# Optimization experiments

Hardware: AMD Instinct MI355X
Metric: run time of the kernel (lower is better)

Reference implementation:

```python
import jax, jax.numpy as jnp
import numpy as np

T_START = 0.0
T_END = 1.0
STEPS = 10
HID = 1024
BATCH = 8192


def setup_inputs() -> dict:
    key = jax.random.key(0)
    ks = jax.random.split(key, 7)
    s1 = 1.0 / np.sqrt(HID + 1)
    s2 = 1.0 / np.sqrt(HID)
    return {
        "h": jax.random.normal(ks[0], (BATCH, HID), dtype=jnp.float32),
        "W1": jax.random.uniform(ks[1], (HID + 1, HID), jnp.float32, -s1, s1),
        "b1": jax.random.uniform(ks[2], (HID,), jnp.float32, -s1, s1),
        "W2": jax.random.uniform(ks[3], (HID, HID), jnp.float32, -s2, s2),
        "b2": jax.random.uniform(ks[4], (HID,), jnp.float32, -s2, s2),
        "W3": jax.random.uniform(ks[5], (HID, HID), jnp.float32, -s2, s2),
        "b3": jax.random.uniform(ks[6], (HID,), jnp.float32, -s2, s2),
    }


def reference(h, W1, b1, W2, b2, W3, b3):
    dt = (T_END - T_START) / STEPS

    def dynamics(t, h):
        # concat(h, t*ones) @ W1 == h @ W1[:-1] + t * W1[-1]; keep explicit concat for clarity
        t_vec = jnp.full((h.shape[0], 1), t, dtype=h.dtype)
        x = jnp.concatenate([h, t_vec], axis=1)
        x = jnp.tanh(x @ W1 + b1)
        x = jnp.tanh(x @ W2 + b2)
        return x @ W3 + b3

    def rk4_step(h, t):
        k1 = dynamics(t, h)
        k2 = dynamics(t + dt / 2, h + dt / 2 * k1)
        k3 = dynamics(t + dt / 2, h + dt / 2 * k2)
        k4 = dynamics(t + dt, h + dt * k3)
        return h + dt / 6 * (k1 + 2 * k2 + 2 * k3 + k4), None

    ts = T_START + dt * jnp.arange(STEPS, dtype=h.dtype)
    h_final, _ = jax.lax.scan(rk4_step, h, ts)
    return h_final
```

## Files before the change

kernel.cpp:

```cpp
#include <hip/hip_runtime.h>


typedef __attribute__((ext_vector_type(8))) __bf16 bf16x8;
typedef __attribute__((ext_vector_type(4))) float f32x4;
typedef __attribute__((ext_vector_type(8))) float f32x8;
typedef __attribute__((ext_vector_type(16))) float f32x16;
typedef __attribute__((ext_vector_type(8))) unsigned short us8;
typedef __attribute__((ext_vector_type(4))) int i32x4;
typedef __attribute__((ext_vector_type(8))) int i32x8;
typedef unsigned short ushort_t;
typedef unsigned char u8;

#define SCALE_ONE  0x7F7F7F7Fu
#define SCALE_INV32 0x7A7A7A7Au

#define GLOAD16(gp, lp) \
  __builtin_amdgcn_global_load_lds((const __attribute__((address_space(1))) unsigned int*)(gp), \
                                   (__attribute__((address_space(3))) unsigned int*)(lp), 16, 0, 0)

__device__ __forceinline__ ushort_t f2bf(float f) {
  union { float f; unsigned u; } v; v.f = f;
  unsigned r = v.u + 0x7fffu + ((v.u >> 16) & 1u);
  return (ushort_t)(r >> 16);
}
__device__ __forceinline__ float b2f(ushort_t u) {
  union { unsigned u; float f; } v; v.u = ((unsigned)u) << 16; return v.f;
}
__device__ __forceinline__ float fast_tanh(float x) {
  float e = __expf(2.0f * x);
  return 1.0f - 2.0f * __builtin_amdgcn_rcpf(e + 1.0f);
}
__device__ __forceinline__ uint2 pack_fp8x8(const float* v) {
  int a = __builtin_amdgcn_cvt_pk_fp8_f32(v[0], v[1], 0, false);
  a = __builtin_amdgcn_cvt_pk_fp8_f32(v[2], v[3], a, true);
  int b = __builtin_amdgcn_cvt_pk_fp8_f32(v[4], v[5], 0, false);
  b = __builtin_amdgcn_cvt_pk_fp8_f32(v[6], v[7], b, true);
  return make_uint2((unsigned)a, (unsigned)b);
}

__global__ void transpose_bf16(const float* __restrict__ in, ushort_t* __restrict__ out) {
  __shared__ float tile[32][33];
  const int bx = blockIdx.x * 32, by = blockIdx.y * 32;
  const int tx = threadIdx.x, ty = threadIdx.y;
#pragma unroll
  for (int i = 0; i < 32; i += 8)
    tile[ty + i][tx] = in[(size_t)(by + ty + i) * 1024 + bx + tx];
  __syncthreads();
#pragma unroll
  for (int i = 0; i < 32; i += 8)
    out[(size_t)(bx + ty + i) * 1024 + by + tx] = f2bf(tile[tx][ty + i]);
}

__global__ void transpose_fp8(const float* __restrict__ in, u8* __restrict__ out) {
  __shared__ float tile[32][33];
  const int bx = blockIdx.x * 32, by = blockIdx.y * 32;
  const int tx = threadIdx.x, ty = threadIdx.y;
#pragma unroll
  for (int i = 0; i < 32; i += 8)
    tile[ty + i][tx] = in[(size_t)(by + ty + i) * 1024 + bx + tx];
  __syncthreads();
#pragma unroll
  for (int i = 0; i < 32; i += 8) {
    const float v = 32.f * tile[tx][ty + i];
    int r = __builtin_amdgcn_cvt_pk_fp8_f32(v, v, 0, false);
    out[(size_t)(bx + ty + i) * 1024 + by + tx] = (u8)(r & 0xFF);
  }
}

__global__ void conv_bf16(const float* __restrict__ in, ushort_t* __restrict__ out) {
  size_t i = ((size_t)blockIdx.x * 256 + threadIdx.x) * 4;
  float4 v = *(const float4*)&in[i];
  ushort4 o;
  o.x = f2bf(v.x); o.y = f2bf(v.y); o.z = f2bf(v.z); o.w = f2bf(v.w);
  *(ushort4*)&out[i] = o;
}

__global__ void c31_kernel(const ushort_t* __restrict__ W1t, const float* __restrict__ b3,
                           float* __restrict__ c31) {
  const int j = blockIdx.x * 256 + threadIdx.x;
  float acc = 0.f;
  for (int c = 0; c < 128; ++c) {
    const us8 w = *(const us8*)&W1t[(size_t)j * 1024 + c * 8];
    const f32x8 b = *(const f32x8*)&b3[c * 8];
#pragma unroll
    for (int e = 0; e < 8; ++e) acc += b2f(w[e]) * b[e];
  }
  c31[j] = acc;
}

template<int MODE>
__global__ void __launch_bounds__(256, 2)
gemm_bf16(const ushort_t* __restrict__ Ag, const ushort_t* __restrict__ Bg,
          const float* __restrict__ bias,
          ushort_t* __restrict__ outb, u8* __restrict__ out8,
          const float* __restrict__ h0f, float* __restrict__ outf)
{
  constexpr int K = 1024, NCOL = 1024, NT = 16;
  constexpr float DT = 0.1f;
  __shared__ __align__(16) ushort_t lds[2][16384];

  const int bid = blockIdx.x;
  const int nb = (int)gridDim.x >> 3;
  const int logical = (bid & 7) * nb + (bid >> 3);
  const int bm0 = (logical >> 3) * 128;
  const int bn0 = (logical & 7) * 128;

  const int tid = threadIdx.x;
  const int w = tid >> 6, l = tid & 63;
  const int wr = w >> 1, wc = w & 1;

  const int srow = l >> 3;
  const int sclog = (l & 7) ^ srow;
  const size_t gA0 = (size_t)(bm0 + w * 32 + srow) * K + sclog * 8;
  const size_t gB0 = (size_t)(bn0 + w * 32 + srow) * K + sclog * 8;
  const int ldsAo = w * 2048 + l * 8;
  const int ldsBo = 8192 + w * 2048 + l * 8;

#define STAGEB(s, t1) do { \
    const ushort_t* ga = Ag + gA0 + (size_t)(t1) * 64; \
    const ushort_t* gb = Bg + gB0 + (size_t)(t1) * 64; \
    GLOAD16(ga,          &lds[s][ldsAo]); \
    GLOAD16(ga + 8 * K,  &lds[s][ldsAo + 512]); \
    GLOAD16(ga + 16 * K, &lds[s][ldsAo + 1024]); \
    GLOAD16(ga + 24 * K, &lds[s][ldsAo + 1536]); \
    GLOAD16(gb,          &lds[s][ldsBo]); \
    GLOAD16(gb + 8 * K,  &lds[s][ldsBo + 512]); \
    GLOAD16(gb + 16 * K, &lds[s][ldsBo + 1024]); \
    GLOAD16(gb + 24 * K, &lds[s][ldsBo + 1536]); } while (0)

  const int r = l & 15, kb = l >> 4, xr = r & 7;
  const int aRow = (wr * 64 + r) * 64;
  const int bRow = 8192 + (wc * 64 + r) * 64;
  const int c0 = ((0 | kb) ^ xr) * 8;
  const int c1 = ((4 | kb) ^ xr) * 8;

  f32x4 acc[4][4];
#pragma unroll
  for (int m = 0; m < 4; ++m)
#pragma unroll
    for (int n = 0; n < 4; ++n) acc[m][n] = (f32x4){0.f, 0.f, 0.f, 0.f};

  STAGEB(0, 0);

  for (int t = 0; t < NT; ++t) {
    const int cur = t & 1;
    __builtin_amdgcn_s_barrier();
    if (t + 1 < NT) {
      STAGEB(cur ^ 1, t + 1);
      asm volatile("s_waitcnt vmcnt(8)" ::: "memory");
    } else {
      asm volatile("s_waitcnt vmcnt(0)" ::: "memory");
    }
    __builtin_amdgcn_s_barrier();
    __builtin_amdgcn_sched_barrier(0);

    const ushort_t* Lb = &lds[cur][0];
    bf16x8 av[4], bv[4];
#pragma unroll
    for (int m = 0; m < 4; ++m) av[m] = *(const bf16x8*)(Lb + aRow + m * 1024 + c0);
#pragma unroll
    for (int n = 0; n < 4; ++n) bv[n] = *(const bf16x8*)(Lb + bRow + n * 1024 + c0);
    __builtin_amdgcn_s_setprio(1);
#pragma unroll
    for (int m = 0; m < 4; ++m)
#pragma unroll
      for (int n = 0; n < 4; ++n)
        acc[m][n] = __builtin_amdgcn_mfma_f32_16x16x32_bf16(av[m], bv[n], acc[m][n], 0, 0, 0);
    __builtin_amdgcn_s_setprio(0);
#pragma unroll
    for (int m = 0; m < 4; ++m) av[m] = *(const bf16x8*)(Lb + aRow + m * 1024 + c1);
#pragma unroll
    for (int n = 0; n < 4; ++n) bv[n] = *(const bf16x8*)(Lb + bRow + n * 1024 + c1);
    __builtin_amdgcn_s_setprio(1);
#pragma unroll
    for (int m = 0; m < 4; ++m)
#pragma unroll
      for (int n = 0; n < 4; ++n)
        acc[m][n] = __builtin_amdgcn_mfma_f32_16x16x32_bf16(av[m], bv[n], acc[m][n], 0, 0, 0);
    __builtin_amdgcn_s_setprio(0);
  }
#undef STAGEB

  __syncthreads();
  ushort_t* C = &lds[0][0];
  const int er = (l >> 4) * 4;
  const int ec = l & 15;
#pragma unroll
  for (int n = 0; n < 4; ++n) {
    const int lc = wc * 64 + n * 16 + ec;
#pragma unroll
    for (int m = 0; m < 4; ++m) {
#pragma unroll
      for (int j = 0; j < 4; ++j) {
        const int lr = wr * 64 + m * 16 + er + j;
        C[lr * 136 + lc] = f2bf(acc[m][n][j]);
      }
    }
  }
  __syncthreads();

  constexpr float DT6 = DT / 6.f;
#pragma unroll
  for (int i = 0; i < 8; ++i) {
    const int chunk = tid + i * 256;
    const int row = chunk >> 4;
    const int cc = chunk & 15;
    const int col0 = bn0 + cc * 8;
    const us8 kv8 = *(const us8*)&C[row * 136 + cc * 8];
    const size_t gidx = (size_t)(bm0 + row) * NCOL + col0;

    if (MODE == 0) {
      float v[8];
#pragma unroll
      for (int e = 0; e < 8; ++e) v[e] = 32.f * b2f(kv8[e]);
      *(uint2*)&out8[gidx] = pack_fp8x8(v);
    } else if (MODE == 1) {
      const f32x8 b = *(const f32x8*)&bias[col0];
      float v[8];
#pragma unroll
      for (int e = 0; e < 8; ++e) v[e] = fast_tanh(b2f(kv8[e]) + b[e]);
      *(us8*)&outb[gidx] = kv8;
      *(uint2*)&out8[gidx] = pack_fp8x8(v);
    } else {
      const f32x8 b = *(const f32x8*)&bias[col0];
      const f32x8 h8 = *(const f32x8*)&h0f[gidx];
      f32x8 o;
#pragma unroll
      for (int e = 0; e < 8; ++e) o[e] = h8[e] + DT6 * b2f(kv8[e]) + b[e];
      *(f32x8*)&outf[gidx] = o;
    }
  }
}

template<int MODE>
__global__ void __launch_bounds__(256, 2)
gemm_fp8(const u8* __restrict__ Ag, const u8* __restrict__ Bg,
         const float* __restrict__ bias, const float* __restrict__ wl,
         const float* __restrict__ c31,
         const ushort_t* __restrict__ hW1r, const ushort_t* __restrict__ GSr,
         u8* __restrict__ out8, ushort_t* __restrict__ bfio, ushort_t* __restrict__ hW1w,
         float p0, float p1, float p2, int flag)
{
  constexpr int NT = 16;
  constexpr float DT = 0.1f, DT6 = DT / 6.f;
  __shared__ __align__(16) u8 bufs[2][16384];
  __shared__ __align__(16) ushort_t Cst[128 * 136];

  const int bid = blockIdx.x;
  const int nb = (int)gridDim.x >> 3;
  const int logical = (bid & 7) * nb + (bid >> 3);
  const int bm0 = (logical >> 3) * 128;
  const int bn0 = (logical & 7) * 128;

  const int tid = threadIdx.x;
  const int w = tid >> 6, l = tid & 63;
  const int wr = w >> 1, wc = w & 1;
  const int l31 = l & 31, kg = l >> 5;

  auto srcoff = [](int slot) -> int {
    int rp = slot >> 3, p = slot & 7, q = p ^ (rp & 7);
    return (2 * rp + (q >> 2)) * 1024 + (q & 3) * 16;
  };
  const int so0 = srcoff(tid), so1 = srcoff(256 + tid);
  const u8* gA = Ag + (size_t)bm0 * 1024;
  const u8* gB = Bg + (size_t)bn0 * 1024;
  const int ld0 = tid * 16, ld1 = 4096 + tid * 16;

#define STAGEF(s, t1) do { \
    GLOAD16(gA + so0 + (t1) * 64, &bufs[s][ld0]); \
    GLOAD16(gA + so1 + (t1) * 64, &bufs[s][ld1]); \
    GLOAD16(gB + so0 + (t1) * 64, &bufs[s][8192 + ld0]); \
    GLOAD16(gB + so1 + (t1) * 64, &bufs[s][8192 + ld1]); } while (0)

  auto ldsAddr = [](int r2, int kc) -> int {
    int q = ((r2 & 1) << 2) | kc; int p = q ^ ((r2 >> 1) & 7);
    return (r2 >> 1) * 128 + p * 16;
  };
  const int kc2 = kg * 2;
  const int ra0 = wr * 64 + l31, ra1 = ra0 + 32;
  const int rb0 = wc * 64 + l31, rb1 = rb0 + 32;
  const int aA00 = ldsAddr(ra0, kc2), aA01 = ldsAddr(ra0, kc2 + 1);
  const int aA10 = ldsAddr(ra1, kc2), aA11 = ldsAddr(ra1, kc2 + 1);
  const int bA00 = 8192 + ldsAddr(rb0, kc2), bA01 = 8192 + ldsAddr(rb0, kc2 + 1);
  const int bA10 = 8192 + ldsAddr(rb1, kc2), bA11 = 8192 + ldsAddr(rb1, kc2 + 1);

  f32x16 acc00, acc01, acc10, acc11;
#pragma unroll
  for (int i = 0; i < 16; ++i) { acc00[i] = 0.f; acc01[i] = 0.f; acc10[i] = 0.f; acc11[i] = 0.f; }

#define LD8(dst, o0, o1) do { \
    i32x4 lo_ = *(const i32x4*)(Lb + (o0)); \
    i32x4 hi_ = *(const i32x4*)(Lb + (o1)); \
    dst = (i32x8){lo_[0], lo_[1], lo_[2], lo_[3], hi_[0], hi_[1], hi_[2], hi_[3]}; } while (0)

  STAGEF(0, 0);

  for (int t = 0; t < NT; ++t) {
    const int cur = t & 1;
    __builtin_amdgcn_s_barrier();
    if (t + 1 < NT) {
      STAGEF(cur ^ 1, t + 1);
      asm volatile("s_waitcnt vmcnt(4)" ::: "memory");
    } else {
      asm volatile("s_waitcnt vmcnt(0)" ::: "memory");
    }
    __builtin_amdgcn_s_barrier();
    __builtin_amdgcn_sched_barrier(0);

    const u8* Lb = &bufs[cur][0];
    i32x8 a0, a1, b0, b1;
    LD8(a0, aA00, aA01);
    LD8(a1, aA10, aA11);
    LD8(b0, bA00, bA01);
    LD8(b1, bA10, bA11);
    __builtin_amdgcn_s_setprio(1);
    acc00 = __builtin_amdgcn_mfma_scale_f32_32x32x64_f8f6f4(a0, b0, acc00, 0, 0, 0, SCALE_ONE, 0, SCALE_INV32);
    acc01 = __builtin_amdgcn_mfma_scale_f32_32x32x64_f8f6f4(a0, b1, acc01, 0, 0, 0, SCALE_ONE, 0, SCALE_INV32);
    acc10 = __builtin_amdgcn_mfma_scale_f32_32x32x64_f8f6f4(a1, b0, acc10, 0, 0, 0, SCALE_ONE, 0, SCALE_INV32);
    acc11 = __builtin_amdgcn_mfma_scale_f32_32x32x64_f8f6f4(a1, b1, acc11, 0, 0, 0, SCALE_ONE, 0, SCALE_INV32);
    __builtin_amdgcn_s_setprio(0);
  }
#undef STAGEF

#define STORE_ACC(A_, mm, nn) do { \
    _Pragma("unroll") \
    for (int reg = 0; reg < 16; ++reg) { \
      const int lrow = wr * 64 + (mm) * 32 + (reg & 3) + 8 * (reg >> 2) + 4 * kg; \
      const int lcol = wc * 64 + (nn) * 32 + l31; \
      Cst[lrow * 136 + lcol] = f2bf(A_[reg]); } } while (0)
  STORE_ACC(acc00, 0, 0);
  STORE_ACC(acc01, 0, 1);
  STORE_ACC(acc10, 1, 0);
  STORE_ACC(acc11, 1, 1);
#undef STORE_ACC
  __syncthreads();

#pragma unroll
  for (int i = 0; i < 8; ++i) {
    const int chunk = tid + i * 256;
    const int row = chunk >> 4;
    const int cc = chunk & 15;
    const int col0 = bn0 + cc * 8;
    const us8 kv8 = *(const us8*)&Cst[row * 136 + cc * 8];
    const size_t gidx = (size_t)(bm0 + row) * 1024 + col0;

    if (MODE == 2) {
      const f32x8 b = *(const f32x8*)&bias[col0];
      float x2v[8];
#pragma unroll
      for (int e = 0; e < 8; ++e) x2v[e] = fast_tanh(b2f(kv8[e]) + b[e]);
      *(uint2*)&out8[gidx] = pack_fp8x8(x2v);
      if (flag) {
        us8 nx;
#pragma unroll
        for (int e = 0; e < 8; ++e) nx[e] = f2bf(x2v[e]);
        *(us8*)&bfio[gidx] = nx;
      } else {
        const us8 xt = *(const us8*)&bfio[gidx];
        us8 nx;
#pragma unroll
        for (int e = 0; e < 8; ++e) nx[e] = f2bf(b2f(xt[e]) + p0 * x2v[e]);
        *(us8*)&bfio[gidx] = nx;
      }
    } else if (MODE == 3) {
      const f32x8 b  = *(const f32x8*)&bias[col0];
      const f32x8 wv = *(const f32x8*)&wl[col0];
      const f32x8 cv = *(const f32x8*)&c31[col0];
      const us8 hw = *(const us8*)&hW1r[gidx];
      float x1v[8]; us8 gs;
      if (flag) {
#pragma unroll
        for (int e = 0; e < 8; ++e) {
          const float g = b2f(kv8[e]);
          gs[e] = f2bf(g);
          x1v[e] = fast_tanh(b2f(hw[e]) + p1 * (g + cv[e]) + b[e] + p2 * wv[e]);
        }
      } else {
        const us8 og = *(const us8*)&bfio[gidx];
#pragma unroll
        for (int e = 0; e < 8; ++e) {
          const float g = b2f(kv8[e]);
          gs[e] = f2bf(b2f(og[e]) + p0 * g);
          x1v[e] = fast_tanh(b2f(hw[e]) + p1 * (g + cv[e]) + b[e] + p2 * wv[e]);
        }
      }
      *(us8*)&bfio[gidx] = gs;
      *(uint2*)&out8[gidx] = pack_fp8x8(x1v);
    } else {
      const f32x8 b  = *(const f32x8*)&bias[col0];
      const f32x8 wv = *(const f32x8*)&wl[col0];
      const f32x8 cv = *(const f32x8*)&c31[col0];
      const us8 hw = *(const us8*)&hW1r[gidx];
      const us8 gs = *(const us8*)&GSr[gidx];
      float x1v[8]; us8 o1;
#pragma unroll
      for (int e = 0; e < 8; ++e) {
        const float hn = b2f(hw[e]) + DT6 * (b2f(gs[e]) + b2f(kv8[e])) + DT * cv[e];
        o1[e] = f2bf(hn);
        x1v[e] = fast_tanh(hn + b[e] + p2 * wv[e]);
      }
      *(us8*)&hW1w[gidx] = o1;
      *(uint2*)&out8[gidx] = pack_fp8x8(x1v);
    }
  }
}

extern "C" void kernel_launch(void* const* d_in, const int* in_sizes, int n_in,
                              void* d_out, int out_size, void* d_ws, size_t ws_size,
                              hipStream_t stream) {
  (void)in_sizes; (void)n_in; (void)out_size; (void)ws_size;
  const float* h_in = (const float*)d_in[0];
  const float* W1   = (const float*)d_in[1];
  const float* b1   = (const float*)d_in[2];
  const float* W2   = (const float*)d_in[3];
  const float* b2   = (const float*)d_in[4];
  const float* W3   = (const float*)d_in[5];
  const float* b3   = (const float*)d_in[6];
  const float* W1last = W1 + (size_t)1024 * 1024;

  char* ws = (char*)d_ws;
  ushort_t* W1t   = (ushort_t*)(ws);
  u8*       W2t8  = (u8*)      (ws + (2ull << 20));
  u8*       Bt318 = (u8*)      (ws + (3ull << 20));
  float*    c31   = (float*)   (ws + (4ull << 20));
  ushort_t* hW1b  = (ushort_t*)(ws + (8ull << 20));
  u8*       x1    = (u8*)      (ws + (24ull << 20));
  u8*       x2    = (u8*)      (ws + (32ull << 20));
  ushort_t* XT    = (ushort_t*)(ws + (40ull << 20));
  ushort_t* GS    = (ushort_t*)d_out;
  ushort_t* hb    = (ushort_t*)d_out;
  float*    OUT   = (float*)d_out;

  const float dt = 0.1f;
  constexpr int GRID = 512, BLK = 256;
  dim3 tb(32, 8), tg(32, 32);

  transpose_bf16<<<tg, tb, 0, stream>>>(W1, W1t);
  transpose_fp8 <<<tg, tb, 0, stream>>>(W2, W2t8);
  conv_bf16<<<1024, 256, 0, stream>>>(W3, XT);
  conv_bf16<<<8192, 256, 0, stream>>>(h_in, hb);
  c31_kernel<<<4, 256, 0, stream>>>(W1t, b3, c31);
  gemm_bf16<0><<<64, BLK, 0, stream>>>(W1t, XT, nullptr, nullptr, Bt318, nullptr, nullptr);
  gemm_bf16<1><<<GRID, BLK, 0, stream>>>(hb, W1t, b1, hW1b, x1, nullptr, nullptr);

  for (int step = 0; step < 10; ++step) {
    const float t0 = step * dt;
    gemm_fp8<2><<<GRID, BLK, 0, stream>>>(x1, W2t8, b2, nullptr, nullptr, nullptr, nullptr,
                                          x2, XT, nullptr, 1.f, 0.f, 0.f, (step == 0));
    gemm_fp8<3><<<GRID, BLK, 0, stream>>>(x2, Bt318, b1, W1last, c31, hW1b, nullptr,
                                          x1, GS, nullptr, 1.f, 0.5f * dt, t0 + 0.5f * dt, 1);
    gemm_fp8<2><<<GRID, BLK, 0, stream>>>(x1, W2t8, b2, nullptr, nullptr, nullptr, nullptr,
                                          x2, XT, nullptr, 2.f, 0.f, 0.f, 0);
    gemm_fp8<3><<<GRID, BLK, 0, stream>>>(x2, Bt318, b1, W1last, c31, hW1b, nullptr,
                                          x1, GS, nullptr, 2.f, 0.5f * dt, t0 + 0.5f * dt, 0);
    gemm_fp8<2><<<GRID, BLK, 0, stream>>>(x1, W2t8, b2, nullptr, nullptr, nullptr, nullptr,
                                          x2, XT, nullptr, 2.f, 0.f, 0.f, 0);
    gemm_fp8<3><<<GRID, BLK, 0, stream>>>(x2, Bt318, b1, W1last, c31, hW1b, nullptr,
                                          x1, GS, nullptr, 2.f, dt, t0 + dt, 0);
    gemm_fp8<2><<<GRID, BLK, 0, stream>>>(x1, W2t8, b2, nullptr, nullptr, nullptr, nullptr,
                                          x2, XT, nullptr, 1.f, 0.f, 0.f, 0);
    if (step < 9) {
      gemm_fp8<4><<<GRID, BLK, 0, stream>>>(x2, Bt318, b1, W1last, c31, hW1b, GS,
                                            x1, nullptr, hW1b, 0.f, 0.f, t0 + dt, 0);
    }
  }

  transpose_bf16<<<tg, tb, 0, stream>>>(W3, W1t);
  gemm_bf16<5><<<GRID, BLK, 0, stream>>>(XT, W1t, b3, nullptr, nullptr, h_in, OUT);
}
```

Measured before the change: 1.703 ms.

## Defer XT accumulation into MODE 4 epilogue and prefetch epilogue operands

```diff
diff --git a/kernel.cpp b/kernel.cpp
--- a/kernel.cpp
+++ b/kernel.cpp
@@ -37,6 +37,15 @@
   b = __builtin_amdgcn_cvt_pk_fp8_f32(v[6], v[7], b, true);
   return make_uint2((unsigned)a, (unsigned)b);
 }
+__device__ __forceinline__ void fp8x4_to_f32(unsigned q, float* o) {
+  o[0] = __builtin_amdgcn_cvt_f32_fp8(q, 0);
+  o[1] = __builtin_amdgcn_cvt_f32_fp8(q, 1);
+  o[2] = __builtin_amdgcn_cvt_f32_fp8(q, 2);
+  o[3] = __builtin_amdgcn_cvt_f32_fp8(q, 3);
+}
+__device__ __forceinline__ void fp8x8_to_f32(uint2 q, float* o) {
+  fp8x4_to_f32(q.x, o); fp8x4_to_f32(q.y, o + 4);
+}
 
 __global__ void transpose_bf16(const float* __restrict__ in, ushort_t* __restrict__ out) {
   __shared__ float tile[32][33];
@@ -86,6 +95,23 @@
     for (int e = 0; e < 8; ++e) acc += b2f(w[e]) * b[e];
   }
   c31[j] = acc;
+}
+
+__global__ void xtfold(const u8* __restrict__ a, const u8* __restrict__ b,
+                       const u8* __restrict__ c, const u8* __restrict__ d,
+                       ushort_t* __restrict__ XT) {
+  const size_t i = ((size_t)blockIdx.x * 256 + threadIdx.x) * 8;
+  float va[8], vb[8], vc[8], vd[8];
+  fp8x8_to_f32(*(const uint2*)&a[i], va);
+  fp8x8_to_f32(*(const uint2*)&b[i], vb);
+  fp8x8_to_f32(*(const uint2*)&c[i], vc);
+  fp8x8_to_f32(*(const uint2*)&d[i], vd);
+  const us8 xo = *(const us8*)&XT[i];
+  us8 xn;
+#pragma unroll
+  for (int e = 0; e < 8; ++e)
+    xn[e] = f2bf(b2f(xo[e]) + va[e] + 2.f * (vb[e] + vc[e]) + vd[e]);
+  *(us8*)&XT[i] = xn;
 }
 
 template<int MODE>
@@ -238,6 +264,7 @@
          const float* __restrict__ bias, const float* __restrict__ wl,
          const float* __restrict__ c31,
          const ushort_t* __restrict__ hW1r, const ushort_t* __restrict__ GSr,
+         const u8* __restrict__ x2a, const u8* __restrict__ x2b, const u8* __restrict__ x2c,
          u8* __restrict__ out8, ushort_t* __restrict__ bfio, ushort_t* __restrict__ hW1w,
          float p0, float p1, float p2, int flag)
 {
@@ -322,6 +349,32 @@
   }
 #undef STAGEF
 
+  us8 hw_pre[8], gs_pre[8];
+  if (MODE == 3 || MODE == 4) {
+#pragma unroll
+    for (int i = 0; i < 8; ++i) {
+      const int chunk = tid + i * 256;
+      const size_t gidx = (size_t)(bm0 + (chunk >> 4)) * 1024 + bn0 + (chunk & 15) * 8;
+      hw_pre[i] = *(const us8*)&hW1r[gidx];
+    }
+  }
+  if (MODE == 3 && !flag) {
+#pragma unroll
+    for (int i = 0; i < 8; ++i) {
+      const int chunk = tid + i * 256;
+      const size_t gidx = (size_t)(bm0 + (chunk >> 4)) * 1024 + bn0 + (chunk & 15) * 8;
+      gs_pre[i] = *(const us8*)&bfio[gidx];
+    }
+  }
+  if (MODE == 4) {
+#pragma unroll
+    for (int i = 0; i < 8; ++i) {
+      const int chunk = tid + i * 256;
+      const size_t gidx = (size_t)(bm0 + (chunk >> 4)) * 1024 + bn0 + (chunk & 15) * 8;
+      gs_pre[i] = *(const us8*)&GSr[gidx];
+    }
+  }
+
 #define STORE_ACC(A_, mm, nn) do { \
     _Pragma("unroll") \
     for (int reg = 0; reg < 16; ++reg) { \
@@ -350,23 +403,11 @@
 #pragma unroll
       for (int e = 0; e < 8; ++e) x2v[e] = fast_tanh(b2f(kv8[e]) + b[e]);
       *(uint2*)&out8[gidx] = pack_fp8x8(x2v);
-      if (flag) {
-        us8 nx;
-#pragma unroll
-        for (int e = 0; e < 8; ++e) nx[e] = f2bf(x2v[e]);
-        *(us8*)&bfio[gidx] = nx;
-      } else {
-        const us8 xt = *(const us8*)&bfio[gidx];
-        us8 nx;
-#pragma unroll
-        for (int e = 0; e < 8; ++e) nx[e] = f2bf(b2f(xt[e]) + p0 * x2v[e]);
-        *(us8*)&bfio[gidx] = nx;
-      }
     } else if (MODE == 3) {
       const f32x8 b  = *(const f32x8*)&bias[col0];
       const f32x8 wv = *(const f32x8*)&wl[col0];
       const f32x8 cv = *(const f32x8*)&c31[col0];
-      const us8 hw = *(const us8*)&hW1r[gidx];
+      const us8 hw = hw_pre[i];
       float x1v[8]; us8 gs;
       if (flag) {
 #pragma unroll
@@ -376,7 +417,7 @@
           x1v[e] = fast_tanh(b2f(hw[e]) + p1 * (g + cv[e]) + b[e] + p2 * wv[e]);
         }
       } else {
-        const us8 og = *(const us8*)&bfio[gidx];
+        const us8 og = gs_pre[i];
 #pragma unroll
         for (int e = 0; e < 8; ++e) {
           const float g = b2f(kv8[e]);
@@ -390,8 +431,25 @@
       const f32x8 b  = *(const f32x8*)&bias[col0];
       const f32x8 wv = *(const f32x8*)&wl[col0];
       const f32x8 cv = *(const f32x8*)&c31[col0];
-      const us8 hw = *(const us8*)&hW1r[gidx];
-      const us8 gs = *(const us8*)&GSr[gidx];
+      const us8 hw = hw_pre[i];
+      const us8 gs = gs_pre[i];
+      float va[8], vb[8], vc[8], vd[8];
+      fp8x8_to_f32(*(const uint2*)&x2a[gidx], va);
+      fp8x8_to_f32(*(const uint2*)&x2b[gidx], vb);
+      fp8x8_to_f32(*(const uint2*)&x2c[gidx], vc);
+      fp8x8_to_f32(*(const uint2*)&Ag[gidx], vd);
+      us8 xtn;
+      if (flag) {
+#pragma unroll
+        for (int e = 0; e < 8; ++e)
+          xtn[e] = f2bf(va[e] + 2.f * (vb[e] + vc[e]) + vd[e]);
+      } else {
+        const us8 xo = *(const us8*)&bfio[gidx];
+#pragma unroll
+        for (int e = 0; e < 8; ++e)
+          xtn[e] = f2bf(b2f(xo[e]) + va[e] + 2.f * (vb[e] + vc[e]) + vd[e]);
+      }
+      *(us8*)&bfio[gidx] = xtn;
       float x1v[8]; us8 o1;
 #pragma unroll
       for (int e = 0; e < 8; ++e) {
@@ -425,8 +483,11 @@
   float*    c31   = (float*)   (ws + (4ull << 20));
   ushort_t* hW1b  = (ushort_t*)(ws + (8ull << 20));
   u8*       x1    = (u8*)      (ws + (24ull << 20));
-  u8*       x2    = (u8*)      (ws + (32ull << 20));
-  ushort_t* XT    = (ushort_t*)(ws + (40ull << 20));
+  u8*       x2s0  = (u8*)      (ws + (32ull << 20));
+  u8*       x2s1  = (u8*)      (ws + (40ull << 20));
+  u8*       x2s2  = (u8*)      (ws + (48ull << 20));
+  u8*       x2s3  = (u8*)      (ws + (56ull << 20));
+  ushort_t* XT    = (ushort_t*)(ws + (64ull << 20));
   ushort_t* GS    = (ushort_t*)d_out;
   ushort_t* hb    = (ushort_t*)d_out;
   float*    OUT   = (float*)d_out;
@@ -446,24 +507,33 @@
   for (int step = 0; step < 10; ++step) {
     const float t0 = step * dt;
     gemm_fp8<2><<<GRID, BLK, 0, stream>>>(x1, W2t8, b2, nullptr, nullptr, nullptr, nullptr,
-                                          x2, XT, nullptr, 1.f, 0.f, 0.f, (step == 0));
-    gemm_fp8<3><<<GRID, BLK, 0, stream>>>(x2, Bt318, b1, W1last, c31, hW1b, nullptr,
-                                          x1, GS, nullptr, 1.f, 0.5f * dt, t0 + 0.5f * dt, 1);
+                                          nullptr, nullptr, nullptr, x2s0, nullptr, nullptr,
+                                          0.f, 0.f, 0.f, 0);
+    gemm_fp8<3><<<GRID, BLK, 0, stream>>>(x2s0, Bt318, b1, W1last, c31, hW1b, nullptr,
+                                          nullptr, nullptr, nullptr, x1, GS, nullptr,
+                                          1.f, 0.5f * dt, t0 + 0.5f * dt, 1);
     gemm_fp8<2><<<GRID, BLK, 0, stream>>>(x1, W2t8, b2, nullptr, nullptr, nullptr, nullptr,
-                                          x2, XT, nullptr, 2.f, 0.f, 0.f, 0);
-    gemm_fp8<3><<<GRID, BLK, 0, stream>>>(x2, Bt318, b1, W1last, c31, hW1b, nullptr,
-                                          x1, GS, nullptr, 2.f, 0.5f * dt, t0 + 0.5f * dt, 0);
+                                          nullptr, nullptr, nullptr, x2s1, nullptr, nullptr,
+                                          0.f, 0.f, 0.f, 0);
+    gemm_fp8<3><<<GRID, BLK, 0, stream>>>(x2s1, Bt318, b1, W1last, c31, hW1b, nullptr,
+                                          nullptr, nullptr, nullptr, x1, GS, nullptr,
+                                          2.f, 0.5f * dt, t0 + 0.5f * dt, 0);
     gemm_fp8<2><<<GRID, BLK, 0, stream>>>(x1, W2t8, b2, nullptr, nullptr, nullptr, nullptr,
-                                          x2, XT, nullptr, 2.f, 0.f, 0.f, 0);
-    gemm_fp8<3><<<GRID, BLK, 0, stream>>>(x2, Bt318, b1, W1last, c31, hW1b, nullptr,
-                                          x1, GS, nullptr, 2.f, dt, t0 + dt, 0);
+                                          nullptr, nullptr, nullptr, x2s2, nullptr, nullptr,
+                                          0.f, 0.f, 0.f, 0);
+    gemm_fp8<3><<<GRID, BLK, 0, stream>>>(x2s2, Bt318, b1, W1last, c31, hW1b, nullptr,
+                                          nullptr, nullptr, nullptr, x1, GS, nullptr,
+                                          2.f, dt, t0 + dt, 0);
     gemm_fp8<2><<<GRID, BLK, 0, stream>>>(x1, W2t8, b2, nullptr, nullptr, nullptr, nullptr,
-                                          x2, XT, nullptr, 1.f, 0.f, 0.f, 0);
+                                          nullptr, nullptr, nullptr, x2s3, nullptr, nullptr,
+                                          0.f, 0.f, 0.f, 0);
     if (step < 9) {
-      gemm_fp8<4><<<GRID, BLK, 0, stream>>>(x2, Bt318, b1, W1last, c31, hW1b, GS,
-                                            x1, nullptr, hW1b, 0.f, 0.f, t0 + dt, 0);
-    }
-  }
+      gemm_fp8<4><<<GRID, BLK, 0, stream>>>(x2s3, Bt318, b1, W1last, c31, hW1b, GS,
+                                            x2s0, x2s1, x2s2, x1, XT, hW1b,
+                                            0.f, 0.f, t0 + dt, (step == 0));
+    }
+  }
+  xtfold<<<4096, 256, 0, stream>>>(x2s0, x2s1, x2s2, x2s3, XT);
 
   transpose_bf16<<<tg, tb, 0, stream>>>(W3, W1t);
   gemm_bf16<5><<<GRID, BLK, 0, stream>>>(XT, W1t, b3, nullptr, nullptr, h_in, OUT);
```

Result: faster. 1.586 ms (-6.9%).
